# Kernel tuning notes

Hardware: AMD Instinct MI355X
Metric: run time of the kernel (lower is better)

## Reference

```python
import jax, jax.numpy as jnp
import numpy as np

N, E, D = 50000, 800000, 128
EPS = 1e-5


def _layernorm(x, g, b):
    m = jnp.mean(x, axis=-1, keepdims=True)
    v = jnp.mean((x - m) ** 2, axis=-1, keepdims=True)
    return (x - m) * jax.lax.rsqrt(v + EPS) * g + b


def setup_inputs() -> dict:
    key = jax.random.key(0)
    ks = jax.random.split(key, 8)
    x = jax.random.normal(ks[0], (N, D), dtype=jnp.float32)
    edge_index = jax.random.randint(ks[1], (2, E), 0, N, dtype=jnp.int64)
    edge_weights = jax.random.uniform(ks[2], (E,), dtype=jnp.float32)
    s = 1.0 / np.sqrt(D)
    W1 = jax.random.uniform(ks[3], (D, D), minval=-s, maxval=s, dtype=jnp.float32)
    b1 = jax.random.uniform(ks[4], (D,), minval=-s, maxval=s, dtype=jnp.float32)
    W2 = jax.random.uniform(ks[5], (D, D), minval=-s, maxval=s, dtype=jnp.float32)
    b2 = jax.random.uniform(ks[6], (D,), minval=-s, maxval=s, dtype=jnp.float32)
    g1 = jnp.ones((D,), jnp.float32); be1 = jnp.zeros((D,), jnp.float32)
    g2 = jnp.ones((D,), jnp.float32); be2 = jnp.zeros((D,), jnp.float32)
    return {"x": x, "edge_index": edge_index, "edge_weights": edge_weights,
            "W1": W1, "b1": b1, "g1": g1, "be1": be1,
            "W2": W2, "b2": b2, "g2": g2, "be2": be2}


def _layer(x, src, dst, ew, W, b, g, be):
    h = jax.nn.relu(x @ W + b)                      # [N, D]
    msg = ew[:, None] * h[src]                      # [E, D] gather
    h = h + jax.ops.segment_sum(msg, dst, num_segments=N)  # scatter-add (matches serial loop)
    return _layernorm(h, g, be)                     # dropout is identity at inference


def reference(x, edge_index, edge_weights, W1, b1, g1, be1, W2, b2, g2, be2):
    src, dst = edge_index[0], edge_index[1]
    x = _layer(x, src, dst, edge_weights, W1, b1, g1, be1)
    x = _layer(x, src, dst, edge_weights, W2, b2, g2, be2)
    return x
```

## Files before the change

kernel.cpp:

```cpp
#include <hip/hip_runtime.h>
#include <hip/hip_bf16.h>


#define D 128
#define SA 8192

typedef __attribute__((ext_vector_type(8))) short short8;
typedef __attribute__((ext_vector_type(4))) float f32x4;
typedef __attribute__((ext_vector_type(2))) unsigned int uint2v;
typedef __attribute__((ext_vector_type(4))) unsigned int uint4v;

__global__ __launch_bounds__(256) void k_prep(const float* __restrict__ W1,
                                              const float* __restrict__ W2,
                                              short* __restrict__ WT1,
                                              short* __restrict__ WT2,
                                              int* __restrict__ bhist, int nb) {
    int b = blockIdx.x;
    if (b < 128) {
        const float* W = (b < 64) ? W1 : W2;
        short* WT = (b < 64) ? WT1 : WT2;
        int i = (b & 63) * 256 + threadIdx.x;
        int k = i >> 7, nn = i & 127;
        WT[nn * 128 + k] = (short)__bfloat16_as_ushort(__float2bfloat16(W[i]));
    } else {
        for (int i = threadIdx.x; i < nb; i += 256) bhist[i] = 0;
    }
}

__global__ __launch_bounds__(1024) void k_bhist(const int* __restrict__ dst, int e,
                                                int n, int nb,
                                                int* __restrict__ bhist) {
    __shared__ int lh[784];
    int tid = threadIdx.x;
    for (int i = tid; i < nb; i += 1024) lh[i] = 0;
    __syncthreads();
    int i0 = blockIdx.x * SA;
#pragma unroll
    for (int k = 0; k < SA / 1024; ++k) {
        int i = i0 + k * 1024 + tid;
        if (i < e) {
            int d = dst[i];
            d = min(max(d, 0), n - 1);
            atomicAdd(&lh[d >> 6], 1);
        }
    }
    __syncthreads();
    for (int i = tid; i < nb; i += 1024)
        if (lh[i]) atomicAdd(&bhist[i], lh[i]);
}

__global__ __launch_bounds__(1024) void k_bscan(const int* __restrict__ bhist, int nb,
                                                int* __restrict__ boff,
                                                int* __restrict__ bcursor) {
    __shared__ int s[1024];
    int t = threadIdx.x;
    int v = (t < nb) ? bhist[t] : 0;
    s[t] = v;
    __syncthreads();
    for (int off = 1; off < 1024; off <<= 1) {
        int u = (t >= off) ? s[t - off] : 0;
        __syncthreads();
        s[t] += u;
        __syncthreads();
    }
    if (t < nb) {
        int ex = s[t] - v;
        boff[t] = ex;
        bcursor[t] = ex;
    }
}

__global__ __launch_bounds__(1024) void k_bfill(const int* __restrict__ src,
                                                const int* __restrict__ dst,
                                                const float* __restrict__ ew, int e,
                                                int n, int nb,
                                                int* __restrict__ bcursor,
                                                uint2v* __restrict__ csr_tmp) {
    __shared__ int lh[784];
    __shared__ int gbase[784];
    int tid = threadIdx.x;
    for (int i = tid; i < nb; i += 1024) lh[i] = 0;
    __syncthreads();
    int i0 = blockIdx.x * SA;
    int bkt[SA / 1024], pos[SA / 1024];
    unsigned pk[SA / 1024];
    float wv[SA / 1024];
#pragma unroll
    for (int k = 0; k < SA / 1024; ++k) {
        int i = i0 + k * 1024 + tid;
        bkt[k] = -1;
        if (i < e) {
            int d = dst[i];
            d = min(max(d, 0), n - 1);
            int s = src[i];
            s = min(max(s, 0), n - 1);
            int b = d >> 6;
            bkt[k] = b;
            pos[k] = atomicAdd(&lh[b], 1);
            pk[k] = (unsigned)s | ((unsigned)(d & 63) << 16);
            wv[k] = ew[i];
        }
    }
    __syncthreads();
    for (int i = tid; i < nb; i += 1024)
        gbase[i] = lh[i] ? atomicAdd(&bcursor[i], lh[i]) : 0;
    __syncthreads();
#pragma unroll
    for (int k = 0; k < SA / 1024; ++k) {
        if (bkt[k] >= 0) {
            int idx = gbase[bkt[k]] + pos[k];
            uint2v en;
            en.x = pk[k];
            en.y = __float_as_uint(wv[k]);
            csr_tmp[idx] = en;
        }
    }
}

#define STG 3072
__global__ __launch_bounds__(256) void k_bfinal(const uint2v* __restrict__ csr_tmp,
                                                const int* __restrict__ boff, int n,
                                                int e, int nb,
                                                int* __restrict__ row_ptr,
                                                uint* __restrict__ csr4) {
    __shared__ uint2v stage[STG];
    __shared__ int dh[64], dcur[64], dscan[64];
    int b = blockIdx.x;
    int tid = threadIdx.x;
    int base = boff[b];
    int endo = (b + 1 < nb) ? boff[b + 1] : e;
    int cnt = endo - base;
    int ndst = min(64, n - b * 64);
    bool st = (cnt <= STG);
    if (tid < 64) { dh[tid] = 0; dcur[tid] = 0; }
    __syncthreads();
    for (int i = tid; i < cnt; i += 256) {
        uint2v en = csr_tmp[base + i];
        if (st) stage[i] = en;
        atomicAdd(&dh[(en.x >> 16) & 63], 1);
    }
    __syncthreads();
    if (tid < 64) {
        int v = dh[tid];
        int incl = v;
#pragma unroll
        for (int off = 1; off < 64; off <<= 1) {
            int u = __shfl_up(incl, off, 64);
            if (tid >= off) incl += u;
        }
        dscan[tid] = incl - v;
        if (tid < ndst) row_ptr[b * 64 + tid] = base + incl - v;
        if (b == nb - 1 && tid == 0) row_ptr[n] = e;
    }
    __syncthreads();
    for (int i = tid; i < cnt; i += 256) {
        uint2v en = st ? stage[i] : csr_tmp[base + i];
        int dlo = (en.x >> 16) & 63;
        int p = atomicAdd(&dcur[dlo], 1);
        uint packed = (en.x & 0xffffu) |
                      ((uint)__bfloat16_as_ushort(
                           __float2bfloat16(__uint_as_float(en.y))) << 16);
        csr4[base + dscan[dlo] + p] = packed;
    }
}

__device__ __forceinline__ short8 cvt8v(f32x4 lo, f32x4 hi) {
    short8 r;
    r[0] = (short)__bfloat16_as_ushort(__float2bfloat16(lo.x));
    r[1] = (short)__bfloat16_as_ushort(__float2bfloat16(lo.y));
    r[2] = (short)__bfloat16_as_ushort(__float2bfloat16(lo.z));
    r[3] = (short)__bfloat16_as_ushort(__float2bfloat16(lo.w));
    r[4] = (short)__bfloat16_as_ushort(__float2bfloat16(hi.x));
    r[5] = (short)__bfloat16_as_ushort(__float2bfloat16(hi.y));
    r[6] = (short)__bfloat16_as_ushort(__float2bfloat16(hi.z));
    r[7] = (short)__bfloat16_as_ushort(__float2bfloat16(hi.w));
    return r;
}

template <int F32IN>
__global__ __launch_bounds__(256) void k_gemm_mfma(const float* __restrict__ xf,
                                                   const short* __restrict__ xb,
                                                   const short* __restrict__ WT,
                                                   const float* __restrict__ bias,
                                                   ushort* __restrict__ hb, int n) {
    int lane = threadIdx.x & 63;
    int w = threadIdx.x >> 6;
    int ln = lane & 15, g = lane >> 4;
    int nt0 = w, nt1 = w + 4;
    short8 bfr0[4], bfr1[4];
#pragma unroll
    for (int kk = 0; kk < 4; ++kk) {
        bfr0[kk] = *(const short8*)(WT + (nt0 * 16 + ln) * 128 + kk * 32 + g * 8);
        bfr1[kk] = *(const short8*)(WT + (nt1 * 16 + ln) * 128 + kk * 32 + g * 8);
    }
    float bv0 = bias[nt0 * 16 + ln];
    float bv1 = bias[nt1 * 16 + ln];

    int ntile = n >> 4;
    int t = blockIdx.x;
    if (t >= ntile) return;

    f32x4 cf[8];
    short8 cb[4];
    auto LOADA = [&](int tt, f32x4* bf, short8* bb) {
        int row = tt * 16 + ln;
        if (F32IN) {
            const f32x4* p = (const f32x4*)(xf + (size_t)row * 128 + g * 8);
#pragma unroll
            for (int kk = 0; kk < 4; ++kk) {
                bf[kk * 2] = p[kk * 8];
                bf[kk * 2 + 1] = p[kk * 8 + 1];
            }
        } else {
            const short8* p = (const short8*)(xb + (size_t)row * 128 + g * 8);
#pragma unroll
            for (int kk = 0; kk < 4; ++kk) bb[kk] = p[kk * 4];
        }
    };
    LOADA(t, cf, cb);
    while (true) {
        int tn = t + (int)gridDim.x;
        f32x4 nf[8];
        short8 nb_[4];
        if (tn < ntile) LOADA(tn, nf, nb_);
        short8 a[4];
        if (F32IN) {
#pragma unroll
            for (int kk = 0; kk < 4; ++kk) a[kk] = cvt8v(cf[kk * 2], cf[kk * 2 + 1]);
        } else {
#pragma unroll
            for (int kk = 0; kk < 4; ++kk) a[kk] = cb[kk];
        }
        f32x4 acc0 = {}, acc1 = {};
#pragma unroll
        for (int kk = 0; kk < 4; ++kk) {
            acc0 = __builtin_amdgcn_mfma_f32_16x16x32_bf16(a[kk], bfr0[kk], acc0, 0, 0, 0);
            acc1 = __builtin_amdgcn_mfma_f32_16x16x32_bf16(a[kk], bfr1[kk], acc1, 0, 0, 0);
        }
        int r0 = t * 16 + g * 4;
#pragma unroll
        for (int r = 0; r < 4; ++r) {
            float v0 = fmaxf(acc0[r] + bv0, 0.0f);
            float v1 = fmaxf(acc1[r] + bv1, 0.0f);
            hb[(size_t)(r0 + r) * 128 + nt0 * 16 + ln] =
                __bfloat16_as_ushort(__float2bfloat16(v0));
            hb[(size_t)(r0 + r) * 128 + nt1 * 16 + ln] =
                __bfloat16_as_ushort(__float2bfloat16(v1));
        }
        if (tn >= ntile) break;
#pragma unroll
        for (int i = 0; i < 8; ++i) cf[i] = nf[i];
#pragma unroll
        for (int i = 0; i < 4; ++i) cb[i] = nb_[i];
        t = tn;
    }
}

__global__ __launch_bounds__(256) void k_aggln(const ushort* __restrict__ hb,
                                               const float* __restrict__ gamma,
                                               const float* __restrict__ beta,
                                               const int* __restrict__ row_ptr,
                                               const uint* __restrict__ csru,
                                               float* __restrict__ out,
                                               uint* __restrict__ xb_out,
                                               int n) {
    int wid = threadIdx.x >> 6;
    int lane = threadIdx.x & 63;
    int node = blockIdx.x * 4 + wid;
    if (node >= n) return;
    int sub = lane >> 4, c = lane & 15;
    const uint4v* hb4 = (const uint4v*)hb;

    float acc[8] = {0.f, 0.f, 0.f, 0.f, 0.f, 0.f, 0.f, 0.f};
    auto ACC8 = [&](uint4v r, float wgt) {
        acc[0] += wgt * __uint_as_float(r.x << 16);
        acc[1] += wgt * __uint_as_float(r.x & 0xffff0000u);
        acc[2] += wgt * __uint_as_float(r.y << 16);
        acc[3] += wgt * __uint_as_float(r.y & 0xffff0000u);
        acc[4] += wgt * __uint_as_float(r.z << 16);
        acc[5] += wgt * __uint_as_float(r.z & 0xffff0000u);
        acc[6] += wgt * __uint_as_float(r.w << 16);
        acc[7] += wgt * __uint_as_float(r.w & 0xffff0000u);
    };

    int beg = row_ptr[node], end = row_ptr[node + 1];
    int j = beg;
    for (; j + 16 <= end; j += 16) {
        uint e0 = csru[j + sub];
        uint e1 = csru[j + 4 + sub];
        uint e2 = csru[j + 8 + sub];
        uint e3 = csru[j + 12 + sub];
        uint4v r0 = hb4[(e0 & 0xffffu) * 16 + c];
        uint4v r1 = hb4[(e1 & 0xffffu) * 16 + c];
        uint4v r2 = hb4[(e2 & 0xffffu) * 16 + c];
        uint4v r3 = hb4[(e3 & 0xffffu) * 16 + c];
        ACC8(r0, __uint_as_float(e0 & 0xffff0000u));
        ACC8(r1, __uint_as_float(e1 & 0xffff0000u));
        ACC8(r2, __uint_as_float(e2 & 0xffff0000u));
        ACC8(r3, __uint_as_float(e3 & 0xffff0000u));
    }
    for (; j < end; j += 4) {
        int jj = j + sub;
        uint ee = csru[jj < end ? jj : (end - 1)];
        float wgt = (jj < end) ? __uint_as_float(ee & 0xffff0000u) : 0.0f;
        uint idx = (jj < end) ? (ee & 0xffffu) : (uint)node;
        uint4v r = hb4[idx * 16 + c];
        ACC8(r, wgt);
    }
#pragma unroll
    for (int i = 0; i < 8; ++i) {
        acc[i] += __shfl_xor(acc[i], 16, 64);
        acc[i] += __shfl_xor(acc[i], 32, 64);
    }
    {
        uint4v s = hb4[(uint)node * 16 + c];
        ACC8(s, 1.0f);
    }
    float sum = acc[0] + acc[1] + acc[2] + acc[3] + acc[4] + acc[5] + acc[6] + acc[7];
#pragma unroll
    for (int m = 1; m < 16; m <<= 1) sum += __shfl_xor(sum, m, 64);
    float mean = sum * (1.0f / 128.0f);
    float d0 = acc[0] - mean, d1 = acc[1] - mean, d2 = acc[2] - mean, d3 = acc[3] - mean;
    float d4 = acc[4] - mean, d5 = acc[5] - mean, d6 = acc[6] - mean, d7 = acc[7] - mean;
    float ss = d0 * d0 + d1 * d1 + d2 * d2 + d3 * d3 + d4 * d4 + d5 * d5 + d6 * d6 + d7 * d7;
#pragma unroll
    for (int m = 1; m < 16; m <<= 1) ss += __shfl_xor(ss, m, 64);
    float rstd = rsqrtf(ss * (1.0f / 128.0f) + 1e-5f);
    f32x4 gA = ((const f32x4*)gamma)[c * 2], gB = ((const f32x4*)gamma)[c * 2 + 1];
    f32x4 bA = ((const f32x4*)beta)[c * 2], bB = ((const f32x4*)beta)[c * 2 + 1];
    f32x4 oA, oB;
    oA.x = d0 * rstd * gA.x + bA.x;
    oA.y = d1 * rstd * gA.y + bA.y;
    oA.z = d2 * rstd * gA.z + bA.z;
    oA.w = d3 * rstd * gA.w + bA.w;
    oB.x = d4 * rstd * gB.x + bB.x;
    oB.y = d5 * rstd * gB.y + bB.y;
    oB.z = d6 * rstd * gB.z + bB.z;
    oB.w = d7 * rstd * gB.w + bB.w;
    if (sub == 0) {
        if (out) {
            f32x4* po = (f32x4*)(out + (size_t)node * 128 + c * 8);
            po[0] = oA;
            po[1] = oB;
        }
        if (xb_out) {
            uint4v u;
            u.x = (uint)__bfloat16_as_ushort(__float2bfloat16(oA.x)) |
                  ((uint)__bfloat16_as_ushort(__float2bfloat16(oA.y)) << 16);
            u.y = (uint)__bfloat16_as_ushort(__float2bfloat16(oA.z)) |
                  ((uint)__bfloat16_as_ushort(__float2bfloat16(oA.w)) << 16);
            u.z = (uint)__bfloat16_as_ushort(__float2bfloat16(oB.x)) |
                  ((uint)__bfloat16_as_ushort(__float2bfloat16(oB.y)) << 16);
            u.w = (uint)__bfloat16_as_ushort(__float2bfloat16(oB.z)) |
                  ((uint)__bfloat16_as_ushort(__float2bfloat16(oB.w)) << 16);
            ((uint4v*)xb_out)[node * 16 + c] = u;
        }
    }
}

extern "C" void kernel_launch(void* const* d_in, const int* in_sizes, int n_in,
                              void* d_out, int out_size, void* d_ws, size_t ws_size,
                              hipStream_t stream) {
    const float* x   = (const float*)d_in[0];
    const int*  eidx = (const int*)d_in[1];
    const float* ew  = (const float*)d_in[2];
    const float* W1  = (const float*)d_in[3];
    const float* b1  = (const float*)d_in[4];
    const float* g1  = (const float*)d_in[5];
    const float* be1 = (const float*)d_in[6];
    const float* W2  = (const float*)d_in[7];
    const float* b2  = (const float*)d_in[8];
    const float* g2  = (const float*)d_in[9];
    const float* be2 = (const float*)d_in[10];
    int n = in_sizes[0] / D;
    int e = in_sizes[2];
    const int* srcp = eidx;
    const int* dstp = eidx + e;

    char* ws = (char*)d_ws;
    size_t off = 0;
    auto alloc = [&](size_t bytes) {
        void* p = ws + off;
        off += (bytes + 255) & ~(size_t)255;
        return p;
    };
    ushort* hb      = (ushort*)alloc((size_t)n * D * sizeof(ushort));
    uint*   xb      = (uint*)alloc((size_t)n * (D / 2) * sizeof(uint));
    int*    row_ptr = (int*)alloc((size_t)(n + 1) * sizeof(int));
    int*    bhist   = (int*)alloc(1024 * sizeof(int));
    int*    boff    = (int*)alloc(1024 * sizeof(int));
    int*    bcursor = (int*)alloc(1024 * sizeof(int));
    short*  WT1     = (short*)alloc(128 * 128 * sizeof(short));
    short*  WT2     = (short*)alloc(128 * 128 * sizeof(short));
    uint2v* csr_tmp = (uint2v*)alloc((size_t)e * sizeof(uint2v));
    uint*   csr4    = (uint*)alloc((size_t)e * sizeof(uint));

    int nb = (n + 63) >> 6;
    int nblk = (e + SA - 1) / SA;

    k_prep<<<129, 256, 0, stream>>>(W1, W2, WT1, WT2, bhist, nb);
    k_bhist<<<nblk, 1024, 0, stream>>>(dstp, e, n, nb, bhist);
    k_bscan<<<1, 1024, 0, stream>>>(bhist, nb, boff, bcursor);
    k_bfill<<<nblk, 1024, 0, stream>>>(srcp, dstp, ew, e, n, nb, bcursor, csr_tmp);
    k_bfinal<<<nb, 256, 0, stream>>>(csr_tmp, boff, n, e, nb, row_ptr, csr4);

    k_gemm_mfma<1><<<512, 256, 0, stream>>>(x, nullptr, WT1, b1, hb, n);
    k_aggln<<<(n + 3) / 4, 256, 0, stream>>>(hb, g1, be1, row_ptr, csr4,
                                             nullptr, xb, n);
    k_gemm_mfma<0><<<512, 256, 0, stream>>>(nullptr, (const short*)xb, WT2, b2, hb, n);
    k_aggln<<<(n + 3) / 4, 256, 0, stream>>>(hb, g2, be2, row_ptr, csr4,
                                             (float*)d_out, nullptr, n);
}
```

Measured before the change: 140.0 us.

## Fold weight prep and histogram zeroing into GEMM, hoist self-row load in aggregation

Drops the separate prep kernel. Each GEMM now reads the fp32 weights directly and converts them to bf16 in registers, and block 0 of the first GEMM zeroes the bucket histogram. The first GEMM launch moves ahead of the CSR build. In the aggregation kernel the self-row load is issued up front and gets an occupancy hint through launch_bounds. The cost is strided scalar weight loads in every GEMM block (512 blocks each convert 128x128 weights) instead of one transposed bf16 copy.

```diff
diff --git a/kernel.cpp b/kernel.cpp
--- a/kernel.cpp
+++ b/kernel.cpp
@@ -9,23 +9,6 @@
 typedef __attribute__((ext_vector_type(4))) float f32x4;
 typedef __attribute__((ext_vector_type(2))) unsigned int uint2v;
 typedef __attribute__((ext_vector_type(4))) unsigned int uint4v;
-
-__global__ __launch_bounds__(256) void k_prep(const float* __restrict__ W1,
-                                              const float* __restrict__ W2,
-                                              short* __restrict__ WT1,
-                                              short* __restrict__ WT2,
-                                              int* __restrict__ bhist, int nb) {
-    int b = blockIdx.x;
-    if (b < 128) {
-        const float* W = (b < 64) ? W1 : W2;
-        short* WT = (b < 64) ? WT1 : WT2;
-        int i = (b & 63) * 256 + threadIdx.x;
-        int k = i >> 7, nn = i & 127;
-        WT[nn * 128 + k] = (short)__bfloat16_as_ushort(__float2bfloat16(W[i]));
-    } else {
-        for (int i = threadIdx.x; i < nb; i += 256) bhist[i] = 0;
-    }
-}
 
 __global__ __launch_bounds__(1024) void k_bhist(const int* __restrict__ dst, int e,
                                                 int n, int nb,
@@ -180,9 +163,13 @@
 template <int F32IN>
 __global__ __launch_bounds__(256) void k_gemm_mfma(const float* __restrict__ xf,
                                                    const short* __restrict__ xb,
-                                                   const short* __restrict__ WT,
+                                                   const float* __restrict__ Wf,
                                                    const float* __restrict__ bias,
-                                                   ushort* __restrict__ hb, int n) {
+                                                   ushort* __restrict__ hb, int n,
+                                                   int* __restrict__ zbuf, int zn) {
+    if (zbuf && blockIdx.x == 0) {
+        for (int i = threadIdx.x; i < zn; i += 256) zbuf[i] = 0;
+    }
     int lane = threadIdx.x & 63;
     int w = threadIdx.x >> 6;
     int ln = lane & 15, g = lane >> 4;
@@ -190,8 +177,15 @@
     short8 bfr0[4], bfr1[4];
 #pragma unroll
     for (int kk = 0; kk < 4; ++kk) {
-        bfr0[kk] = *(const short8*)(WT + (nt0 * 16 + ln) * 128 + kk * 32 + g * 8);
-        bfr1[kk] = *(const short8*)(WT + (nt1 * 16 + ln) * 128 + kk * 32 + g * 8);
+        short8 f0, f1;
+#pragma unroll
+        for (int i = 0; i < 8; ++i) {
+            int k = kk * 32 + g * 8 + i;
+            f0[i] = (short)__bfloat16_as_ushort(__float2bfloat16(Wf[k * 128 + nt0 * 16 + ln]));
+            f1[i] = (short)__bfloat16_as_ushort(__float2bfloat16(Wf[k * 128 + nt1 * 16 + ln]));
+        }
+        bfr0[kk] = f0;
+        bfr1[kk] = f1;
     }
     float bv0 = bias[nt0 * 16 + ln];
     float bv1 = bias[nt1 * 16 + ln];
@@ -256,20 +250,22 @@
     }
 }
 
-__global__ __launch_bounds__(256) void k_aggln(const ushort* __restrict__ hb,
-                                               const float* __restrict__ gamma,
-                                               const float* __restrict__ beta,
-                                               const int* __restrict__ row_ptr,
-                                               const uint* __restrict__ csru,
-                                               float* __restrict__ out,
-                                               uint* __restrict__ xb_out,
-                                               int n) {
+__global__ __launch_bounds__(256, 8) void k_aggln(const ushort* __restrict__ hb,
+                                                  const float* __restrict__ gamma,
+                                                  const float* __restrict__ beta,
+                                                  const int* __restrict__ row_ptr,
+                                                  const uint* __restrict__ csru,
+                                                  float* __restrict__ out,
+                                                  uint* __restrict__ xb_out,
+                                                  int n) {
     int wid = threadIdx.x >> 6;
     int lane = threadIdx.x & 63;
     int node = blockIdx.x * 4 + wid;
     if (node >= n) return;
     int sub = lane >> 4, c = lane & 15;
     const uint4v* hb4 = (const uint4v*)hb;
+
+    uint4v selfrow = hb4[(uint)node * 16 + c];
 
     float acc[8] = {0.f, 0.f, 0.f, 0.f, 0.f, 0.f, 0.f, 0.f};
     auto ACC8 = [&](uint4v r, float wgt) {
@@ -312,10 +308,7 @@
         acc[i] += __shfl_xor(acc[i], 16, 64);
         acc[i] += __shfl_xor(acc[i], 32, 64);
     }
-    {
-        uint4v s = hb4[(uint)node * 16 + c];
-        ACC8(s, 1.0f);
-    }
+    ACC8(selfrow, 1.0f);
     float sum = acc[0] + acc[1] + acc[2] + acc[3] + acc[4] + acc[5] + acc[6] + acc[7];
 #pragma unroll
     for (int m = 1; m < 16; m <<= 1) sum += __shfl_xor(sum, m, 64);
@@ -390,24 +383,23 @@
     int*    bhist   = (int*)alloc(1024 * sizeof(int));
     int*    boff    = (int*)alloc(1024 * sizeof(int));
     int*    bcursor = (int*)alloc(1024 * sizeof(int));
-    short*  WT1     = (short*)alloc(128 * 128 * sizeof(short));
-    short*  WT2     = (short*)alloc(128 * 128 * sizeof(short));
     uint2v* csr_tmp = (uint2v*)alloc((size_t)e * sizeof(uint2v));
     uint*   csr4    = (uint*)alloc((size_t)e * sizeof(uint));
 
     int nb = (n + 63) >> 6;
     int nblk = (e + SA - 1) / SA;
 
-    k_prep<<<129, 256, 0, stream>>>(W1, W2, WT1, WT2, bhist, nb);
+    k_gemm_mfma<1><<<512, 256, 0, stream>>>(x, nullptr, W1, b1, hb, n, bhist, nb);
+
     k_bhist<<<nblk, 1024, 0, stream>>>(dstp, e, n, nb, bhist);
     k_bscan<<<1, 1024, 0, stream>>>(bhist, nb, boff, bcursor);
     k_bfill<<<nblk, 1024, 0, stream>>>(srcp, dstp, ew, e, n, nb, bcursor, csr_tmp);
     k_bfinal<<<nb, 256, 0, stream>>>(csr_tmp, boff, n, e, nb, row_ptr, csr4);
 
-    k_gemm_mfma<1><<<512, 256, 0, stream>>>(x, nullptr, WT1, b1, hb, n);
     k_aggln<<<(n + 3) / 4, 256, 0, stream>>>(hb, g1, be1, row_ptr, csr4,
                                              nullptr, xb, n);
-    k_gemm_mfma<0><<<512, 256, 0, stream>>>(nullptr, (const short*)xb, WT2, b2, hb, n);
+    k_gemm_mfma<0><<<512, 256, 0, stream>>>(nullptr, (const short*)xb, W2, b2, hb, n,
+                                            nullptr, 0);
     k_aggln<<<(n + 3) / 4, 256, 0, stream>>>(hb, g2, be2, row_ptr, csr4,
                                              (float*)d_out, nullptr, n);
 }
```

After: 134.0 us, median of 2. 4.3% less time.
